# Kernel optimization log

Measured on AMD Instinct MI355X. Metric: run time of the kernel, lower is better.

Reference implementation:

```python
import jax, jax.numpy as jnp
import numpy as np

HEADS = 8
DIM_HEAD = 8  # TransMIL passes heads as dim_head to NystromLayer
INNER = HEADS * DIM_HEAD  # 64
LANDMARKS = 256
PINV_ITERS = 6
HID = 512
IN_DIM = 1024
N_TOKENS = 19600


def layernorm(x, g, b, eps=1e-5):
    mu = x.mean(-1, keepdims=True)
    var = ((x - mu) ** 2).mean(-1, keepdims=True)
    return (x - mu) / jnp.sqrt(var + eps) * g + b


def moore_penrose_pinv(a, iters=PINV_ITERS):
    # a: [b, h, m, m]
    abs_a = jnp.abs(a)
    z = jnp.swapaxes(a, -1, -2) / (jnp.max(abs_a.sum(-1)) * jnp.max(abs_a.sum(-2)))
    I = jnp.eye(a.shape[-1], dtype=a.dtype)
    for _ in range(iters):
        az = a @ z
        z = 0.25 * z @ (13.0 * I - az @ (15.0 * I - az @ (7.0 * I - az)))
    return z


def dwconv2d(x, w, b, pad_h, pad_w):
    # x: [B,C,H,W], w: [C,1,kh,kw] depthwise
    y = jax.lax.conv_general_dilated(
        x, w, (1, 1), [(pad_h, pad_h), (pad_w, pad_w)],
        dimension_numbers=('NCHW', 'OIHW', 'NCHW'), feature_group_count=x.shape[1])
    if b is not None:
        y = y + b[None, :, None, None]
    return y


def nystrom_attention(x, qkv_w, out_w, out_b, res_w):
    b, n, _ = x.shape
    m = LANDMARKS
    pad = (m - n % m) % m
    xp = jnp.pad(x, ((0, 0), (pad, 0), (0, 0)))  # pad at the FRONT (as in lucidrains)
    n_p = n + pad
    qkv = xp @ qkv_w  # [b, n_p, 3*inner]
    q, k, v = jnp.split(qkv, 3, axis=-1)
    to_heads = lambda t: t.reshape(b, n_p, HEADS, DIM_HEAD).transpose(0, 2, 1, 3)
    q, k, v = to_heads(q), to_heads(k), to_heads(v)  # [b,h,n_p,d]
    q = q * (DIM_HEAD ** -0.5)
    l = n_p // m  # segment length per landmark
    q_l = q.reshape(b, HEADS, m, l, DIM_HEAD).mean(3)  # [b,h,m,d]
    k_l = k.reshape(b, HEADS, m, l, DIM_HEAD).mean(3)
    attn1 = jax.nn.softmax(jnp.einsum('bhid,bhjd->bhij', q, k_l), -1)    # [b,h,n_p,m]
    attn2 = jax.nn.softmax(jnp.einsum('bhid,bhjd->bhij', q_l, k_l), -1)  # [b,h,m,m]
    attn3 = jax.nn.softmax(jnp.einsum('bhid,bhjd->bhij', q_l, k), -1)    # [b,h,m,n_p]
    out = (attn1 @ moore_penrose_pinv(attn2)) @ (attn3 @ v)  # [b,h,n_p,d]
    # residual depthwise conv over sequence dim: Conv2d(heads, heads, (33,1), padding=(16,0), groups=heads)
    out = out + dwconv2d(v, res_w, None, 16, 0)
    out = out.transpose(0, 2, 1, 3).reshape(b, n_p, INNER)
    out = out @ out_w + out_b
    return out[:, -n:]


def ppeg(x, H, W, w7, b7, w5, b5, w3, b3):
    B, _, C = x.shape
    cls, feat = x[:, :1], x[:, 1:]
    f = feat.transpose(0, 2, 1).reshape(B, C, H, W)
    y = f + dwconv2d(f, w7, b7, 3, 3) + dwconv2d(f, w5, b5, 2, 2) + dwconv2d(f, w3, b3, 1, 1)
    y = y.reshape(B, C, H * W).transpose(0, 2, 1)
    return jnp.concatenate([cls, y], axis=1)


def transmil_forward(x, fc1_w, fc1_b, cls_token,
                     l1_norm_g, l1_norm_b, l1_qkv_w, l1_out_w, l1_out_b, l1_res_w,
                     l2_norm_g, l2_norm_b, l2_qkv_w, l2_out_w, l2_out_b, l2_res_w,
                     ppeg7_w, ppeg7_b, ppeg5_w, ppeg5_b, ppeg3_w, ppeg3_b,
                     norm_g, norm_b):
    h = jax.nn.gelu(x @ fc1_w + fc1_b, approximate=False)  # [1, N, HID]
    N = h.shape[1]
    side = int(np.ceil(np.sqrt(N)))
    add = side * side - N
    h = jnp.concatenate([h, h[:, :add]], axis=1)
    cls = jnp.broadcast_to(cls_token, (h.shape[0], 1, h.shape[2]))
    h = jnp.concatenate([cls, h], axis=1)
    h = h + nystrom_attention(layernorm(h, l1_norm_g, l1_norm_b), l1_qkv_w, l1_out_w, l1_out_b, l1_res_w)
    h = ppeg(h, side, side, ppeg7_w, ppeg7_b, ppeg5_w, ppeg5_b, ppeg3_w, ppeg3_b)
    h = h + nystrom_attention(layernorm(h, l2_norm_g, l2_norm_b), l2_qkv_w, l2_out_w, l2_out_b, l2_res_w)
    return layernorm(h, norm_g, norm_b)[:, 0]  # [1, HID]


def setup_inputs() -> dict:
    key = jax.random.key(0)
    ks = jax.random.split(key, 16)
    s = 0.02
    inp = {
        'x': jax.random.normal(ks[0], (1, N_TOKENS, IN_DIM), jnp.float32),
        'fc1_w': jax.random.normal(ks[1], (IN_DIM, HID), jnp.float32) * s,
        'fc1_b': jnp.zeros((HID,), jnp.float32),
        'cls_token': jax.random.normal(ks[2], (1, 1, HID), jnp.float32),
        'l1_norm_g': jnp.ones((HID,), jnp.float32),
        'l1_norm_b': jnp.zeros((HID,), jnp.float32),
        'l1_qkv_w': jax.random.normal(ks[3], (HID, 3 * INNER), jnp.float32) * s,
        'l1_out_w': jax.random.normal(ks[4], (INNER, HID), jnp.float32) * s,
        'l1_out_b': jnp.zeros((HID,), jnp.float32),
        'l1_res_w': jax.random.normal(ks[5], (HEADS, 1, 33, 1), jnp.float32) * 0.05,
        'l2_norm_g': jnp.ones((HID,), jnp.float32),
        'l2_norm_b': jnp.zeros((HID,), jnp.float32),
        'l2_qkv_w': jax.random.normal(ks[6], (HID, 3 * INNER), jnp.float32) * s,
        'l2_out_w': jax.random.normal(ks[7], (INNER, HID), jnp.float32) * s,
        'l2_out_b': jnp.zeros((HID,), jnp.float32),
        'l2_res_w': jax.random.normal(ks[8], (HEADS, 1, 33, 1), jnp.float32) * 0.05,
        'ppeg7_w': jax.random.normal(ks[9], (HID, 1, 7, 7), jnp.float32) * 0.05,
        'ppeg7_b': jnp.zeros((HID,), jnp.float32),
        'ppeg5_w': jax.random.normal(ks[10], (HID, 1, 5, 5), jnp.float32) * 0.05,
        'ppeg5_b': jnp.zeros((HID,), jnp.float32),
        'ppeg3_w': jax.random.normal(ks[11], (HID, 1, 3, 3), jnp.float32) * 0.05,
        'ppeg3_b': jnp.zeros((HID,), jnp.float32),
        'norm_g': jnp.ones((HID,), jnp.float32),
        'norm_b': jnp.zeros((HID,), jnp.float32),
    }
    return inp


def reference(x, fc1_w, fc1_b, cls_token,
              l1_norm_g, l1_norm_b, l1_qkv_w, l1_out_w, l1_out_b, l1_res_w,
              l2_norm_g, l2_norm_b, l2_qkv_w, l2_out_w, l2_out_b, l2_res_w,
              ppeg7_w, ppeg7_b, ppeg5_w, ppeg5_b, ppeg3_w, ppeg3_b,
              norm_g, norm_b):
    return transmil_forward(x, fc1_w, fc1_b, cls_token,
                            l1_norm_g, l1_norm_b, l1_qkv_w, l1_out_w, l1_out_b, l1_res_w,
                            l2_norm_g, l2_norm_b, l2_qkv_w, l2_out_w, l2_out_b, l2_res_w,
                            ppeg7_w, ppeg7_b, ppeg5_w, ppeg5_b, ppeg3_w, ppeg3_b,
                            norm_g, norm_b)
```

## Files before the change

### kernel.cpp

```cpp
#include <hip/hip_runtime.h>

namespace {

constexpr int NP   = 19712;
constexpr int NT   = 19601;
constexpr int NPIX = 19600;
constexpr int HD   = 512;
constexpr int ID   = 1024;
constexpr int NH   = 8;
constexpr int DH   = 8;
constexpr int NL   = 256;
constexpr int PADR = 111;
constexpr int SIDE = 140;
constexpr int A3CHK = 256;
constexpr int A3NB  = NP / A3CHK;

constexpr int PTW = 16, PTH = 16, PCC = 16;
constexpr int PHW = PTW + 6, PHH = PTH + 6;
constexpr int PSLOT = 20;

typedef __attribute__((ext_vector_type(8))) short bf16x8;
typedef __attribute__((ext_vector_type(4))) float f32x4;

#define F4MAD(a, s, v) { (a).x += (s)*(v).x; (a).y += (s)*(v).y; (a).z += (s)*(v).z; (a).w += (s)*(v).w; }
#define F4FMA(a, ww, v) { (a).x += (ww).x*(v).x; (a).y += (ww).y*(v).y; (a).z += (ww).z*(v).z; (a).w += (ww).w*(v).w; }

#define GLOAD16(gptr, lptr) \
    __builtin_amdgcn_global_load_lds((const __attribute__((address_space(1))) void*)(gptr), \
                                     (__attribute__((address_space(3))) void*)(lptr), 16, 0, 0)

__device__ inline short f2bf(float f) {
    union { float f; unsigned u; } v; v.f = f;
    unsigned r = v.u + 0x7fffu + ((v.u >> 16) & 1u);
    return (short)(r >> 16);
}

__global__ void castX(const float* __restrict__ src, short* __restrict__ dst)
{
    size_t c = (size_t)blockIdx.x * 256 + threadIdx.x;
    const float4 x0 = *(const float4*)&src[c * 8];
    const float4 x1 = *(const float4*)&src[c * 8 + 4];
    bf16x8 p;
    p[0] = f2bf(x0.x); p[1] = f2bf(x0.y); p[2] = f2bf(x0.z); p[3] = f2bf(x0.w);
    p[4] = f2bf(x1.x); p[5] = f2bf(x1.y); p[6] = f2bf(x1.z); p[7] = f2bf(x1.w);
    *(bf16x8*)&dst[c * 8] = p;
}

__global__ void castT(const float* __restrict__ src, short* __restrict__ dst, int R, int C)
{
    __shared__ float t[32][33];
    const int tx = threadIdx.x & 31, ty = threadIdx.x >> 5;
    const int c0 = blockIdx.x * 32, r0 = blockIdx.y * 32;
    #pragma unroll
    for (int j = 0; j < 4; ++j)
        t[ty + 8 * j][tx] = src[(size_t)(r0 + ty + 8 * j) * C + c0 + tx];
    __syncthreads();
    #pragma unroll
    for (int j = 0; j < 4; ++j)
        dst[(size_t)(c0 + ty + 8 * j) * R + r0 + tx] = f2bf(t[tx][ty + 8 * j]);
}

__global__ __launch_bounds__(256) void gemm_fc1(const short* __restrict__ Xb,
                                                const short* __restrict__ Wt,
                                                const float* __restrict__ bias,
                                                float* __restrict__ out)
{
    __shared__ __align__(16) short As[2][128 * 32];
    __shared__ __align__(16) short Bs[2][128 * 32];
    const int tid  = threadIdx.x;
    const int col0 = blockIdx.x * 128;
    const int row0 = blockIdx.y * 128;
    const int wave = tid >> 6, lane = tid & 63;
    const int quad = lane >> 4, l16 = lane & 15;
    const int m_base = (wave >> 1) * 64, n_base = (wave & 1) * 64;
    const int kch = (quad ^ ((l16 >> 1) & 3)) * 8;
    f32x4 acc[4][4] = {};

    int    aldo[2];
    size_t agoff[2], bgoff[2];
    #pragma unroll
    for (int i = 0; i < 2; ++i) {
        int slot = i * 256 + wave * 64 + lane;
        int row  = slot >> 2;
        int g    = (slot & 3) ^ ((slot >> 3) & 3);
        aldo[i]  = slot * 8;
        agoff[i] = (size_t)(row0 + row) * ID + g * 8;
        bgoff[i] = (size_t)(col0 + row) * ID + g * 8;
    }
    auto stage = [&](int b, int k0) {
        #pragma unroll
        for (int i = 0; i < 2; ++i) {
            GLOAD16(&Xb[agoff[i] + k0], &As[b][aldo[i]]);
            GLOAD16(&Wt[bgoff[i] + k0], &Bs[b][aldo[i]]);
        }
    };

    stage(0, 0);
    __syncthreads();
    #pragma unroll 1
    for (int t = 0; t < 32; ++t) {
        const int cur = t & 1;
        if (t < 31) stage(cur ^ 1, (t + 1) * 32);
        bf16x8 af[4], bfr[4];
        #pragma unroll
        for (int i = 0; i < 4; ++i) {
            af[i]  = *(const bf16x8*)&As[cur][(m_base + i * 16 + l16) * 32 + kch];
            bfr[i] = *(const bf16x8*)&Bs[cur][(n_base + i * 16 + l16) * 32 + kch];
        }
        #pragma unroll
        for (int mi = 0; mi < 4; ++mi)
            #pragma unroll
            for (int ni = 0; ni < 4; ++ni)
                acc[mi][ni] = __builtin_amdgcn_mfma_f32_16x16x32_bf16(af[mi], bfr[ni], acc[mi][ni], 0, 0, 0);
        __syncthreads();
    }
    #pragma unroll
    for (int mi = 0; mi < 4; ++mi) {
        #pragma unroll
        for (int r = 0; r < 4; ++r) {
            int gr = row0 + m_base + mi * 16 + quad * 4 + r;
            if (gr >= NPIX) continue;
            #pragma unroll
            for (int ni = 0; ni < 4; ++ni) {
                int gc = col0 + n_base + ni * 16 + l16;
                float v = acc[mi][ni][r] + bias[gc];
                v = 0.5f * v * (1.f + erff(v * 0.70710678118654752f));
                out[(size_t)(gr + 1) * HD + gc] = v;
            }
        }
    }
}

__global__ __launch_bounds__(256) void gemm_qkv(const short* __restrict__ xpB,
                                                const short* __restrict__ Wt,
                                                float* __restrict__ qh,
                                                float* __restrict__ kh,
                                                float* __restrict__ vh)
{
    __shared__ __align__(16) short As[2][128 * 32];
    __shared__ __align__(16) short Bs[2][64 * 32];
    const int tid  = threadIdx.x;
    const int col0 = blockIdx.x * 64;
    const int row0 = blockIdx.y * 128;
    const int wave = tid >> 6, lane = tid & 63;
    const int quad = lane >> 4, l16 = lane & 15;
    const int m_base = (wave >> 1) * 64, n_base = (wave & 1) * 32;
    const int kch = (quad ^ ((l16 >> 1) & 3)) * 8;
    f32x4 acc[4][2] = {};

    int    aldo[2];
    size_t agoff[2];
    #pragma unroll
    for (int i = 0; i < 2; ++i) {
        int slot = i * 256 + wave * 64 + lane;
        int row  = slot >> 2;
        int g    = (slot & 3) ^ ((slot >> 3) & 3);
        aldo[i]  = slot * 8;
        agoff[i] = (size_t)(row0 + row) * HD + g * 8;
    }
    int bldo; size_t bgoff;
    {
        int slot = wave * 64 + lane;
        int row  = slot >> 2;
        int g    = (slot & 3) ^ ((slot >> 3) & 3);
        bldo  = slot * 8;
        bgoff = (size_t)(col0 + row) * HD + g * 8;
    }
    auto stage = [&](int b, int k0) {
        #pragma unroll
        for (int i = 0; i < 2; ++i)
            GLOAD16(&xpB[agoff[i] + k0], &As[b][aldo[i]]);
        GLOAD16(&Wt[bgoff + k0], &Bs[b][bldo]);
    };

    stage(0, 0);
    __syncthreads();
    #pragma unroll 1
    for (int t = 0; t < 16; ++t) {
        const int cur = t & 1;
        if (t < 15) stage(cur ^ 1, (t + 1) * 32);
        bf16x8 af[4], bfr[2];
        #pragma unroll
        for (int i = 0; i < 4; ++i)
            af[i] = *(const bf16x8*)&As[cur][(m_base + i * 16 + l16) * 32 + kch];
        #pragma unroll
        for (int i = 0; i < 2; ++i)
            bfr[i] = *(const bf16x8*)&Bs[cur][(n_base + i * 16 + l16) * 32 + kch];
        #pragma unroll
        for (int mi = 0; mi < 4; ++mi)
            #pragma unroll
            for (int ni = 0; ni < 2; ++ni)
                acc[mi][ni] = __builtin_amdgcn_mfma_f32_16x16x32_bf16(af[mi], bfr[ni], acc[mi][ni], 0, 0, 0);
        __syncthreads();
    }
    const int which = blockIdx.x;
    float* dst = (which == 0) ? qh : (which == 1) ? kh : vh;
    const float scale = (which == 0) ? 0.35355339059327373f : 1.f;
    #pragma unroll
    for (int mi = 0; mi < 4; ++mi) {
        #pragma unroll
        for (int r = 0; r < 4; ++r) {
            int gr = row0 + m_base + mi * 16 + quad * 4 + r;
            #pragma unroll
            for (int ni = 0; ni < 2; ++ni) {
                int n = n_base + ni * 16 + l16;
                int hh = n >> 3, d = n & 7;
                dst[((size_t)hh * NP + gr) * DH + d] = acc[mi][ni][r] * scale;
            }
        }
    }
}

__global__ void cls_init(const float* __restrict__ cls, float* __restrict__ h)
{
    int t = blockIdx.x * 256 + threadIdx.x;
    if (t < HD) h[t] = cls[t];
}

__global__ void copy512(const float* __restrict__ src, float* __restrict__ dst)
{
    dst[threadIdx.x] = src[threadIdx.x];
}

__global__ __launch_bounds__(256) void ln_pad(const float* __restrict__ h,
                                              const float* __restrict__ g,
                                              const float* __restrict__ b,
                                              short* __restrict__ xp)
{
    const int wave = threadIdx.x >> 6, lane = threadIdx.x & 63;
    const int row = blockIdx.x * 4 + wave;
    short* dst = xp + (size_t)row * HD + lane * 8;
    if (row < PADR) {
        bf16x8 z = {};
        *(bf16x8*)dst = z;
        return;
    }
    const float* src = h + (size_t)(row - PADR) * HD + lane * 8;
    float4 v0 = *(const float4*)src;
    float4 v1 = *(const float4*)(src + 4);
    float v[8] = {v0.x, v0.y, v0.z, v0.w, v1.x, v1.y, v1.z, v1.w};
    float s = 0.f;
    #pragma unroll
    for (int i = 0; i < 8; ++i) s += v[i];
    #pragma unroll
    for (int o = 1; o < 64; o <<= 1) s += __shfl_xor(s, o);
    float mu = s * (1.f / HD);
    float ss = 0.f;
    #pragma unroll
    for (int i = 0; i < 8; ++i) { float d = v[i] - mu; ss += d * d; }
    #pragma unroll
    for (int o = 1; o < 64; o <<= 1) ss += __shfl_xor(ss, o);
    float inv = rsqrtf(ss * (1.f / HD) + 1e-5f);
    float4 g0 = *(const float4*)&g[lane * 8];
    float4 g1 = *(const float4*)&g[lane * 8 + 4];
    float4 b0 = *(const float4*)&b[lane * 8];
    float4 b1 = *(const float4*)&b[lane * 8 + 4];
    float gg[8] = {g0.x, g0.y, g0.z, g0.w, g1.x, g1.y, g1.z, g1.w};
    float bb[8] = {b0.x, b0.y, b0.z, b0.w, b1.x, b1.y, b1.z, b1.w};
    bf16x8 o;
    #pragma unroll
    for (int i = 0; i < 8; ++i) o[i] = f2bf((v[i] - mu) * inv * gg[i] + bb[i]);
    *(bf16x8*)dst = o;
}

__global__ void landmarks(const float* __restrict__ qh, const float* __restrict__ kh,
                          float* __restrict__ ql, float* __restrict__ kl)
{
    int idx = blockIdx.x * 256 + threadIdx.x;
    int sel = idx >> 14;
    int rem = idx & 16383;
    int h = rem >> 11;
    int i = (rem >> 3) & 255;
    int d = rem & 7;
    const float* src = sel ? kh : qh;
    size_t base = ((size_t)h * NP + (size_t)i * 77) * DH + d;
    float s = 0.f;
    for (int j = 0; j < 77; ++j) s += src[base + (size_t)j * DH];
    (sel ? kl : ql)[((size_t)h * NL + i) * DH + d] = s * (1.f / 77.f);
}

__global__ void attn2_softmax(const float* __restrict__ ql, const float* __restrict__ kl,
                              float* __restrict__ a)
{
    const int i = blockIdx.x, h = blockIdx.y, j = threadIdx.x;
    __shared__ float sq[8];
    __shared__ float red[256];
    if (j < 8) sq[j] = ql[((size_t)h * NL + i) * DH + j];
    __syncthreads();
    const float* kr = kl + ((size_t)h * NL + j) * DH;
    float s = 0.f;
    #pragma unroll
    for (int d = 0; d < 8; ++d) s += sq[d] * kr[d];
    float e = __expf(s);
    red[j] = e;
    __syncthreads();
    for (int off = 128; off > 0; off >>= 1) {
        if (j < off) red[j] += red[j + off];
        __syncthreads();
    }
    a[((size_t)h * NL + i) * NL + j] = e / red[0];
}

__global__ void pinv_norms(const float* __restrict__ a, float* __restrict__ part)
{
    const int h = blockIdx.x & 7;
    const int mode = blockIdx.x >> 3;
    const int tid = threadIdx.x;
    const float* ah = a + (size_t)h * NL * NL;
    float s = 0.f;
    if (mode == 0) { for (int j = 0; j < NL; ++j) s += fabsf(ah[tid * NL + j]); }
    else           { for (int i = 0; i < NL; ++i) s += fabsf(ah[i * NL + tid]); }
    __shared__ float red[256];
    red[tid] = s;
    __syncthreads();
    for (int off = 128; off > 0; off >>= 1) {
        if (tid < off) red[tid] = fmaxf(red[tid], red[tid + off]);
        __syncthreads();
    }
    if (tid == 0) part[mode * 8 + h] = red[0];
}

__global__ void z0_init(const float* __restrict__ a, const float* __restrict__ part,
                        float* __restrict__ z)
{
    float s1 = part[0], s2 = part[8];
    #pragma unroll
    for (int h = 1; h < 8; ++h) { s1 = fmaxf(s1, part[h]); s2 = fmaxf(s2, part[8 + h]); }
    float inv = 1.f / (s1 * s2);
    int idx = blockIdx.x * 256 + threadIdx.x;
    int h = idx >> 16;
    int rem = idx & 65535;
    int i = rem >> 8, j = rem & 255;
    z[idx] = a[((size_t)h * NL + j) * NL + i] * inv;
}

__global__ void mm256(const float* __restrict__ A, const float* __restrict__ B,
                      float* __restrict__ D)
{
    const int h = blockIdx.z;
    const float* Ah = A + (size_t)h * NL * NL;
    const float* Bh = B + (size_t)h * NL * NL;
    float* Dh = D + (size_t)h * NL * NL;
    __shared__ __align__(16) float As[16][36];
    __shared__ __align__(16) float Bs[16][68];
    const int tid = threadIdx.x;
    const int tx = tid & 15, ty = tid >> 4;
    const int row0 = blockIdx.x * 32;
    const int col0 = blockIdx.y * 64;
    float acc[2][4] = {};
    const int ar = tid >> 3;
    const int ak = (tid & 7) * 2;
    const int bk = tid >> 4;
    const int bj = (tid & 15) * 4;
    for (int k0 = 0; k0 < NL; k0 += 16) {
        float2 av = *(const float2*)&Ah[(size_t)(row0 + ar) * NL + k0 + ak];
        As[ak][ar] = av.x; As[ak + 1][ar] = av.y;
        *(float4*)&Bs[bk][bj] = *(const float4*)&Bh[(size_t)(k0 + bk) * NL + col0 + bj];
        __syncthreads();
        #pragma unroll
        for (int k = 0; k < 16; ++k) {
            float2 a = *(const float2*)&As[k][ty * 2];
            float4 b = *(const float4*)&Bs[k][tx * 4];
            acc[0][0] += a.x * b.x; acc[0][1] += a.x * b.y; acc[0][2] += a.x * b.z; acc[0][3] += a.x * b.w;
            acc[1][0] += a.y * b.x; acc[1][1] += a.y * b.y; acc[1][2] += a.y * b.z; acc[1][3] += a.y * b.w;
        }
        __syncthreads();
    }
    #pragma unroll
    for (int r = 0; r < 2; ++r) {
        int gr = row0 + ty * 2 + r;
        #pragma unroll
        for (int c = 0; c < 4; ++c)
            Dh[(size_t)gr * NL + col0 + tx * 4 + c] = acc[r][c];
    }
}

__global__ __launch_bounds__(256) void mmF(const float* __restrict__ S,
                                           const float* __restrict__ w,
                                           float* __restrict__ wn,
                                           const float* __restrict__ yin,
                                           float* __restrict__ yout)
{
    const int h = blockIdx.z;
    const int tid = threadIdx.x;
    if (blockIdx.y == 4) {
        __shared__ float yL[NL * 9];
        __shared__ float tL[NL * 9];
        __shared__ float uL[NL * 9];
        const int s = blockIdx.x;
        const float* yh = yin + (size_t)h * NL * DH;
        #pragma unroll
        for (int i = 0; i < 8; ++i) {
            int idx = tid + 256 * i;
            yL[(idx >> 3) * 9 + (idx & 7)] = yh[idx];
        }
        __syncthreads();
        const float* wr = w + ((size_t)h * NL + tid) * NL;
        float t1[8] = {};
        for (int j = 0; j < NL; j += 4) {
            float4 wv = *(const float4*)&wr[j];
            #pragma unroll
            for (int d = 0; d < 8; ++d)
                t1[d] += wv.x * yL[j * 9 + d] + wv.y * yL[(j + 1) * 9 + d]
                       + wv.z * yL[(j + 2) * 9 + d] + wv.w * yL[(j + 3) * 9 + d];
        }
        #pragma unroll
        for (int d = 0; d < 8; ++d) {
            tL[tid * 9 + d] = t1[d];
            uL[tid * 9 + d] = 7.f * yL[tid * 9 + d] - t1[d];
        }
        __syncthreads();
        const int r = s * 32 + (tid >> 3), d = tid & 7;
        const float* Sr = S + ((size_t)h * NL + r) * NL;
        float acc = 13.f * yL[r * 9 + d] - 15.f * tL[r * 9 + d];
        for (int j = 0; j < NL; j += 4) {
            float4 sv = *(const float4*)&Sr[j];
            acc += sv.x * uL[j * 9 + d] + sv.y * uL[(j + 1) * 9 + d]
                 + sv.z * uL[(j + 2) * 9 + d] + sv.w * uL[(j + 3) * 9 + d];
        }
        yout[((size_t)h * NL + r) * DH + d] = acc;
        return;
    }
    const float* Sh = S + (size_t)h * NL * NL;
    const float* wh = w + (size_t)h * NL * NL;
    float* Dh = wn + (size_t)h * NL * NL;
    __shared__ __align__(16) float As[16][36];
    __shared__ __align__(16) float Bs[16][68];
    const int tx = tid & 15, ty = tid >> 4;
    const int row0 = blockIdx.x * 32;
    const int col0 = blockIdx.y * 64;
    float acc[2][4] = {};
    const int ar = tid >> 3;
    const int ak = (tid & 7) * 2;
    const int bk = tid >> 4;
    const int bj = (tid & 15) * 4;
    for (int k0 = 0; k0 < NL; k0 += 16) {
        float2 av = *(const float2*)&Sh[(size_t)(row0 + ar) * NL + k0 + ak];
        As[ak][ar] = av.x; As[ak + 1][ar] = av.y;
        size_t bo = (size_t)(k0 + bk) * NL + col0 + bj;
        float4 bw = *(const float4*)&wh[bo];
        float4 bs = *(const float4*)&Sh[bo];
        Bs[bk][bj]     = 7.f * bw.x - bs.x;
        Bs[bk][bj + 1] = 7.f * bw.y - bs.y;
        Bs[bk][bj + 2] = 7.f * bw.z - bs.z;
        Bs[bk][bj + 3] = 7.f * bw.w - bs.w;
        __syncthreads();
        #pragma unroll
        for (int k = 0; k < 16; ++k) {
            float2 a = *(const float2*)&As[k][ty * 2];
            float4 b = *(const float4*)&Bs[k][tx * 4];
            acc[0][0] += a.x * b.x; acc[0][1] += a.x * b.y; acc[0][2] += a.x * b.z; acc[0][3] += a.x * b.w;
            acc[1][0] += a.y * b.x; acc[1][1] += a.y * b.y; acc[1][2] += a.y * b.z; acc[1][3] += a.y * b.w;
        }
        __syncthreads();
    }
    #pragma unroll
    for (int r = 0; r < 2; ++r) {
        int gr = row0 + ty * 2 + r;
        #pragma unroll
        for (int c = 0; c < 4; ++c) {
            int gc = col0 + tx * 4 + c;
            size_t o = (size_t)gr * NL + gc;
            Dh[o] = 0.25f * (13.f * wh[o] - 15.f * Sh[o] + acc[r][c]);
        }
    }
}

__global__ __launch_bounds__(256) void yiter(const float* __restrict__ w,
                                             const float* __restrict__ S,
                                             const float* __restrict__ yin,
                                             float* __restrict__ yout)
{
    const int s = blockIdx.x, h = blockIdx.y, tid = threadIdx.x;
    __shared__ float yL[NL * 9];
    __shared__ float tL[NL * 9];
    __shared__ float uL[NL * 9];
    const float* yh = yin + (size_t)h * NL * DH;
    #pragma unroll
    for (int i = 0; i < 8; ++i) {
        int idx = tid + 256 * i;
        yL[(idx >> 3) * 9 + (idx & 7)] = yh[idx];
    }
    __syncthreads();
    const float* wr = w + ((size_t)h * NL + tid) * NL;
    float t1[8] = {};
    for (int j = 0; j < NL; j += 4) {
        float4 wv = *(const float4*)&wr[j];
        #pragma unroll
        for (int d = 0; d < 8; ++d)
            t1[d] += wv.x * yL[j * 9 + d] + wv.y * yL[(j + 1) * 9 + d]
                   + wv.z * yL[(j + 2) * 9 + d] + wv.w * yL[(j + 3) * 9 + d];
    }
    #pragma unroll
    for (int d = 0; d < 8; ++d) {
        tL[tid * 9 + d] = t1[d];
        uL[tid * 9 + d] = 7.f * yL[tid * 9 + d] - t1[d];
    }
    __syncthreads();
    const int r = s * 32 + (tid >> 3), d = tid & 7;
    const float* Sr = S + ((size_t)h * NL + r) * NL;
    float acc = 13.f * yL[r * 9 + d] - 15.f * tL[r * 9 + d];
    for (int j = 0; j < NL; j += 4) {
        float4 sv = *(const float4*)&Sr[j];
        acc += sv.x * uL[j * 9 + d] + sv.y * uL[(j + 1) * 9 + d]
             + sv.z * uL[(j + 2) * 9 + d] + sv.w * uL[(j + 3) * 9 + d];
    }
    yout[((size_t)h * NL + r) * DH + d] = acc;
}

__global__ void polyv(const float* __restrict__ M, const float* __restrict__ vin,
                      float* __restrict__ vout, float scale)
{
    const int h = blockIdx.y;
    __shared__ float vs[NL * DH];
    const int tid = threadIdx.x;
    const float* vh = vin + (size_t)h * NL * DH;
    #pragma unroll
    for (int i = 0; i < 8; ++i) vs[tid + 256 * i] = vh[tid + 256 * i];
    __syncthreads();
    const int row = blockIdx.x * 32 + (tid >> 3);
    const int d = tid & 7;
    const float* Mr = M + ((size_t)h * NL + row) * NL;
    float acc = 0.f;
    #pragma unroll 4
    for (int j = 0; j < NL; j += 4) {
        float4 m = *(const float4*)&Mr[j];
        acc += m.x * vs[j * 8 + d]      + m.y * vs[j * 8 + 8 + d]
             + m.z * vs[j * 8 + 16 + d] + m.w * vs[j * 8 + 24 + d];
    }
    vout[((size_t)h * NL + row) * DH + d] = acc * scale;
}

__global__ __launch_bounds__(256) void attn3v(const float* __restrict__ kh,
                                              const float* __restrict__ vh,
                                              const float* __restrict__ ql,
                                              float* __restrict__ part)
{
    const int ck = blockIdx.x, h = blockIdx.y, tid = threadIdx.x;
    __shared__ __align__(16) float4 kv[A3CHK][4];
    const float* kb = kh + ((size_t)h * NP + (size_t)ck * A3CHK) * DH;
    const float* vb = vh + ((size_t)h * NP + (size_t)ck * A3CHK) * DH;
    #pragma unroll
    for (int i = 0; i < 2; ++i) {
        int idx = tid + 256 * i;
        int t = idx >> 1, p = idx & 1;
        kv[t][p]     = *(const float4*)&kb[t * 8 + p * 4];
        kv[t][2 + p] = *(const float4*)&vb[t * 8 + p * 4];
    }
    float q[8];
    const float* qp = ql + ((size_t)h * NL + tid) * DH;
    #pragma unroll
    for (int d = 0; d < 8; ++d) q[d] = qp[d];
    __syncthreads();
    float den = 0.f;
    float4 a0 = make_float4(0.f, 0.f, 0.f, 0.f);
    float4 a1 = make_float4(0.f, 0.f, 0.f, 0.f);
    #pragma unroll 4
    for (int t = 0; t < A3CHK; ++t) {
        float4 k0 = kv[t][0], k1 = kv[t][1];
        float s = q[0] * k0.x + q[1] * k0.y + q[2] * k0.z + q[3] * k0.w
                + q[4] * k1.x + q[5] * k1.y + q[6] * k1.z + q[7] * k1.w;
        float e = __expf(s);
        den += e;
        float4 v0 = kv[t][2], v1 = kv[t][3];
        F4MAD(a0, e, v0); F4MAD(a1, e, v1);
    }
    float* p = part + (((size_t)h * A3NB + ck) * NL + tid) * 9;
    p[0] = den;
    p[1] = a0.x; p[2] = a0.y; p[3] = a0.z; p[4] = a0.w;
    p[5] = a1.x; p[6] = a1.y; p[7] = a1.z; p[8] = a1.w;
}

__global__ void attn3v_merge(const float* __restrict__ part, float* __restrict__ y)
{
    const int h = blockIdx.x;
    const int i = blockIdx.y * 32 + (threadIdx.x >> 3);
    const int d = threadIdx.x & 7;
    float acc = 0.f, den = 0.f;
    const float* p = part + ((size_t)h * A3NB * NL + i) * 9;
    for (int ck = 0; ck < A3NB; ++ck) {
        const float* q = p + (size_t)ck * NL * 9;
        den += q[0];
        acc += q[1 + d];
    }
    y[((size_t)h * NL + i) * DH + d] = acc / den;
}

__global__ __launch_bounds__(256) void attn1_conv(const float* __restrict__ qh,
                                                  const float* __restrict__ vh,
                                                  const float* __restrict__ klg,
                                                  const float* __restrict__ zwg,
                                                  const float* __restrict__ rw,
                                                  float* __restrict__ aout)
{
    const int h = blockIdx.y;
    __shared__ __align__(16) float kl[NL * DH];
    __shared__ __align__(16) float zw[NL * DH];
    const int tid = threadIdx.x;
    #pragma unroll
    for (int q = 0; q < 8; ++q) {
        kl[tid + 256 * q] = klg[(size_t)h * NL * DH + tid + 256 * q];
        zw[tid + 256 * q] = zwg[(size_t)h * NL * DH + tid + 256 * q];
    }
    __syncthreads();
    const int r = blockIdx.x * 256 + tid;
    if (r >= NT) return;
    const int t = r + PADR;
    const float* qp = qh + ((size_t)h * NP + t) * DH;
    float4 q0 = *(const float4*)qp;
    float4 q1 = *(const float4*)(qp + 4);
    float den = 0.f;
    float4 acc0 = make_float4(0.f, 0.f, 0.f, 0.f);
    float4 acc1 = make_float4(0.f, 0.f, 0.f, 0.f);
    #pragma unroll 4
    for (int i = 0; i < NL; ++i) {
        float4 k0 = *(const float4*)&kl[i * 8];
        float4 k1 = *(const float4*)&kl[i * 8 + 4];
        float s = q0.x * k0.x + q0.y * k0.y + q0.z * k0.z + q0.w * k0.w
                + q1.x * k1.x + q1.y * k1.y + q1.z * k1.z + q1.w * k1.w;
        float e = __expf(s);
        den += e;
        float4 z0 = *(const float4*)&zw[i * 8];
        float4 z1 = *(const float4*)&zw[i * 8 + 4];
        F4MAD(acc0, e, z0); F4MAD(acc1, e, z1);
    }
    float inv = 1.f / den;
    const float* vb = vh + (size_t)h * NP * DH;
    float4 c0 = make_float4(0.f, 0.f, 0.f, 0.f);
    float4 c1 = make_float4(0.f, 0.f, 0.f, 0.f);
    #pragma unroll
    for (int j = 0; j < 33; ++j) {
        int tp = t - 16 + j;
        if (tp >= NP) continue;
        float wv = rw[h * 33 + j];
        float4 v0 = *(const float4*)&vb[(size_t)tp * 8];
        float4 v1 = *(const float4*)&vb[(size_t)tp * 8 + 4];
        F4MAD(c0, wv, v0); F4MAD(c1, wv, v1);
    }
    float* op = aout + (size_t)r * 64 + h * 8;
    *(float4*)op = make_float4(acc0.x * inv + c0.x, acc0.y * inv + c0.y,
                               acc0.z * inv + c0.z, acc0.w * inv + c0.w);
    *(float4*)(op + 4) = make_float4(acc1.x * inv + c1.x, acc1.y * inv + c1.y,
                                     acc1.z * inv + c1.z, acc1.w * inv + c1.w);
}

__global__ void outproj(const float* __restrict__ aout, const float* __restrict__ W,
                        const float* __restrict__ bias, float* __restrict__ h)
{
    const int r0 = blockIdx.x * 16;
    const int tid = threadIdx.x;
    __shared__ float ao[16][64];
    #pragma unroll
    for (int s = 0; s < 2; ++s) {
        int idx = tid + s * 512;
        int rr = idx >> 6, kk = idx & 63;
        int gr = r0 + rr;
        ao[rr][kk] = (gr < NT) ? aout[(size_t)gr * 64 + kk] : 0.f;
    }
    __syncthreads();
    float acc[16] = {};
    for (int k = 0; k < 64; ++k) {
        float wv = W[(size_t)k * HD + tid];
        #pragma unroll
        for (int r = 0; r < 16; ++r) acc[r] += ao[r][k] * wv;
    }
    float bv = bias[tid];
    #pragma unroll
    for (int r = 0; r < 16; ++r) {
        int gr = r0 + r;
        if (gr < NT) h[(size_t)gr * HD + tid] += acc[r] + bv;
    }
}

__global__ void ppeg_wprep(const float* __restrict__ w7, const float* __restrict__ b7,
                           const float* __restrict__ w5, const float* __restrict__ b5,
                           const float* __restrict__ w3, const float* __restrict__ b3,
                           float* __restrict__ wc, float* __restrict__ bsum)
{
    int idx = blockIdx.x * 256 + threadIdx.x;
    if (idx < HD * 49) {
        int c = idx / 49, t = idx - c * 49;
        int dy = t / 7 - 3, dx = t % 7 - 3;
        float v = w7[idx];
        if (dy >= -2 && dy <= 2 && dx >= -2 && dx <= 2) v += w5[c * 25 + (dy + 2) * 5 + (dx + 2)];
        if (dy >= -1 && dy <= 1 && dx >= -1 && dx <= 1) v += w3[c * 9 + (dy + 1) * 3 + (dx + 1)];
        if (t == 24) v += 1.f;
        wc[idx] = v;
    } else if (idx < HD * 49 + HD) {
        int c = idx - HD * 49;
        bsum[c] = b7[c] + b5[c] + b3[c];
    }
}

__global__ __launch_bounds__(256) void ppeg_direct(const float* __restrict__ hin,
                                                   const float* __restrict__ wc,
                                                   const float* __restrict__ bsum,
                                                   float* __restrict__ hout)
{
    __shared__ __align__(16) float in_sh[PHH * PHW * PSLOT];
    __shared__ float wL[49 * PCC];
    const int tid = threadIdx.x;
    const int tx0 = blockIdx.x * PTW;
    const int ty0 = blockIdx.y * PTH;
    const int c0  = blockIdx.z * PCC;
    for (int i = tid; i < 49 * PCC; i += 256) {
        int c = i / 49, tap = i - c * 49;
        wL[tap * PCC + c] = wc[(size_t)(c0 + c) * 49 + tap];
    }
    for (int idx = tid; idx < PHH * PHW * 4; idx += 256) {
        int pos = idx >> 2, q = idx & 3;
        int ly = pos / PHW, lx = pos - ly * PHW;
        int gy = ty0 - 3 + ly, gx = tx0 - 3 + lx;
        float4 v = make_float4(0.f, 0.f, 0.f, 0.f);
        if (gy >= 0 && gy < SIDE && gx >= 0 && gx < SIDE)
            v = *(const float4*)&hin[(size_t)(1 + gy * SIDE + gx) * HD + c0 + q * 4];
        *(float4*)&in_sh[pos * PSLOT + q * 4] = v;
    }
    __syncthreads();
    const int y  = tid >> 4;
    const int x4 = (tid >> 2) & 3;
    const int c4 = tid & 3;
    const int xb = x4 * 4;
    float4 acc[4] = {make_float4(0.f,0.f,0.f,0.f), make_float4(0.f,0.f,0.f,0.f),
                     make_float4(0.f,0.f,0.f,0.f), make_float4(0.f,0.f,0.f,0.f)};
    #pragma unroll 1
    for (int dy = 0; dy < 7; ++dy) {
        float4 row[10];
        #pragma unroll
        for (int k = 0; k < 10; ++k)
            row[k] = *(const float4*)&in_sh[((y + dy) * PHW + xb + k) * PSLOT + c4 * 4];
        #pragma unroll
        for (int dx = 0; dx < 7; ++dx) {
            float4 wv = *(const float4*)&wL[(dy * 7 + dx) * PCC + c4 * 4];
            #pragma unroll
            for (int xi = 0; xi < 4; ++xi) F4FMA(acc[xi], wv, row[xi + dx]);
        }
    }
    const int gy = ty0 + y;
    if (gy >= SIDE) return;
    float4 bv = *(const float4*)&bsum[c0 + c4 * 4];
    #pragma unroll
    for (int xi = 0; xi < 4; ++xi) {
        int gx = tx0 + xb + xi;
        if (gx >= SIDE) continue;
        float4 o = make_float4(acc[xi].x + bv.x, acc[xi].y + bv.y,
                               acc[xi].z + bv.z, acc[xi].w + bv.w);
        *(float4*)&hout[(size_t)(1 + gy * SIDE + gx) * HD + c0 + c4 * 4] = o;
    }
}

__global__ void final_ln(const float* __restrict__ h, const float* __restrict__ g,
                         const float* __restrict__ b, float* __restrict__ out)
{
    const int tid = threadIdx.x;
    float v0 = h[tid], v1 = h[tid + 256];
    __shared__ float red[256];
    red[tid] = v0 + v1;
    __syncthreads();
    for (int off = 128; off > 0; off >>= 1) {
        if (tid < off) red[tid] += red[tid + off];
        __syncthreads();
    }
    float mu = red[0] * (1.f / HD);
    __syncthreads();
    float d0 = v0 - mu, d1 = v1 - mu;
    red[tid] = d0 * d0 + d1 * d1;
    __syncthreads();
    for (int off = 128; off > 0; off >>= 1) {
        if (tid < off) red[tid] += red[tid + off];
        __syncthreads();
    }
    float inv = rsqrtf(red[0] * (1.f / HD) + 1e-5f);
    out[tid]       = d0 * inv * g[tid] + b[tid];
    out[tid + 256] = d1 * inv * g[tid + 256] + b[tid + 256];
}

}

extern "C" void kernel_launch(void* const* d_in, const int* in_sizes, int n_in,
                              void* d_out, int out_size, void* d_ws, size_t ws_size,
                              hipStream_t stream)
{
    const float* x      = (const float*)d_in[0];
    const float* fc1_w  = (const float*)d_in[1];
    const float* fc1_b  = (const float*)d_in[2];
    const float* cls    = (const float*)d_in[3];
    const float* l1_g   = (const float*)d_in[4];
    const float* l1_bb  = (const float*)d_in[5];
    const float* l1_qkv = (const float*)d_in[6];
    const float* l1_ow  = (const float*)d_in[7];
    const float* l1_ob  = (const float*)d_in[8];
    const float* l1_rw  = (const float*)d_in[9];
    const float* l2_g   = (const float*)d_in[10];
    const float* l2_bb  = (const float*)d_in[11];
    const float* l2_qkv = (const float*)d_in[12];
    const float* l2_ow  = (const float*)d_in[13];
    const float* l2_ob  = (const float*)d_in[14];
    const float* l2_rw  = (const float*)d_in[15];
    const float* p7w    = (const float*)d_in[16];
    const float* p7b    = (const float*)d_in[17];
    const float* p5w    = (const float*)d_in[18];
    const float* p5b    = (const float*)d_in[19];
    const float* p3w    = (const float*)d_in[20];
    const float* p3b    = (const float*)d_in[21];
    const float* ng     = (const float*)d_in[22];
    const float* nb     = (const float*)d_in[23];
    float* out = (float*)d_out;

    char* ws = (char*)d_ws;
    size_t off = 0;
    auto alloc = [&](size_t bytes) {
        char* p = ws + off;
        off += (bytes + 255) & ~(size_t)255;
        return (void*)p;
    };
    float* bufA = (float*)alloc((size_t)NP * HD * 4);
    float* bufB = (float*)alloc((size_t)NP * HD * 4);
    float* qh   = (float*)alloc((size_t)NH * NP * DH * 4);
    float* kh   = (float*)alloc((size_t)NH * NP * DH * 4);
    float* vh   = (float*)alloc((size_t)NH * NP * DH * 4);
    float* aout = (float*)alloc((size_t)NP * 64 * 4);
    float* ql   = (float*)alloc((size_t)NH * NL * DH * 4);
    float* klm  = (float*)alloc((size_t)NH * NL * DH * 4);
    float* ybuf = (float*)alloc((size_t)NH * NL * DH * 4);
    float* ybuf2= (float*)alloc((size_t)NH * NL * DH * 4);
    float* zwb  = (float*)alloc((size_t)NH * NL * DH * 4);
    float* a2   = (float*)alloc((size_t)NH * NL * NL * 4);
    float* zb0  = (float*)alloc((size_t)NH * NL * NL * 4);
    float* azb  = (float*)alloc((size_t)NH * NL * NL * 4);
    float* tb   = (float*)alloc((size_t)NH * NL * NL * 4);
    float* ub   = (float*)alloc((size_t)NH * NL * NL * 4);
    float* part = (float*)alloc(256);
    float* a3p  = (float*)alloc((size_t)NH * A3NB * NL * 9 * 4);
    float* wcomb = (float*)alloc((size_t)HD * 49 * 4);
    float* bsum  = (float*)alloc((size_t)HD * 4);
    short* wt1   = (short*)alloc((size_t)HD * ID * 2);
    short* wtq   = (short*)alloc((size_t)192 * HD * 2);
    short* xb    = (short*)alloc((size_t)NP * ID * 2);
    short* xpB   = (short*)alloc((size_t)NP * HD * 2);
    (void)ws_size; (void)in_sizes; (void)n_in; (void)out_size;

    castX<<<(NPIX * ID / 8) / 256, 256, 0, stream>>>(x, xb);
    castT<<<dim3(HD / 32, ID / 32), 256, 0, stream>>>(fc1_w, wt1, ID, HD);
    gemm_fc1<<<dim3(4, 154), 256, 0, stream>>>(xb, wt1, fc1_b, bufA);
    cls_init<<<2, 256, 0, stream>>>(cls, bufA);

    auto attention = [&](float* hbuf, const float* lg, const float* lb,
                         const float* qkvw, const float* ow, const float* ob,
                         const float* rw) {
        ln_pad<<<NP / 4, 256, 0, stream>>>(hbuf, lg, lb, xpB);
        castT<<<dim3(192 / 32, HD / 32), 256, 0, stream>>>(qkvw, wtq, HD, 192);
        gemm_qkv<<<dim3(3, 154), 256, 0, stream>>>(xpB, wtq, qh, kh, vh);
        landmarks<<<128, 256, 0, stream>>>(qh, kh, ql, klm);
        attn2_softmax<<<dim3(NL, NH), 256, 0, stream>>>(ql, klm, a2);
        pinv_norms<<<16, 256, 0, stream>>>(a2, part);
        z0_init<<<2048, 256, 0, stream>>>(a2, part, zb0);
        attn3v<<<dim3(A3NB, NH), 256, 0, stream>>>(kh, vh, ql, a3p);
        attn3v_merge<<<dim3(NH, 8), 256, 0, stream>>>(a3p, ybuf);
        mm256<<<dim3(8, 4, 8), 256, 0, stream>>>(a2, zb0, azb);
        float* wc = azb;
        float* wn = tb;
        float* yc = ybuf;
        float* yn = ybuf2;
        for (int it = 0; it < 6; ++it) {
            mm256<<<dim3(8, 4, 8), 256, 0, stream>>>(wc, wc, ub);
            if (it < 5) {
                mmF<<<dim3(8, 5, 8), 256, 0, stream>>>(ub, wc, wn, yc, yn);
                { float* t = yc; yc = yn; yn = t; }
                { float* t = wc; wc = wn; wn = t; }
            } else {
                yiter<<<dim3(8, 8), 256, 0, stream>>>(wc, ub, yc, yn);
                { float* t = yc; yc = yn; yn = t; }
            }
        }
        polyv<<<dim3(8, NH), 256, 0, stream>>>(zb0, yc, zwb, 2.44140625e-4f);
        attn1_conv<<<dim3(77, NH), 256, 0, stream>>>(qh, vh, klm, zwb, rw, aout);
        outproj<<<(NT + 15) / 16, 512, 0, stream>>>(aout, ow, ob, hbuf);
    };

    attention(bufA, l1_g, l1_bb, l1_qkv, l1_ow, l1_ob, l1_rw);

    ppeg_wprep<<<(HD * 49 + HD + 255) / 256, 256, 0, stream>>>(p7w, p7b, p5w, p5b, p3w, p3b,
                                                               wcomb, bsum);
    copy512<<<1, 512, 0, stream>>>(bufA, bufB);
    ppeg_direct<<<dim3((SIDE + PTW - 1) / PTW, (SIDE + PTH - 1) / PTH, HD / PCC),
                  256, 0, stream>>>(bufA, wcomb, bsum, bufB);

    attention(bufB, l2_g, l2_bb, l2_qkv, l2_ow, l2_ob, l2_rw);
    final_ln<<<1, 256, 0, stream>>>(bufB, ng, nb, out);
}
```

Measured before the change: 1.032 ms.

## Retile QKV GEMM over all outputs and fold pinv init transpose into consumers

The QKV projection GEMM now has each block cover 64 rows and all 192 output columns, so each activation tile is read once instead of three times. The pseudo-inverse setup drops the explicit transposed z0 matrix. It assumes softmax rows sum to one and are non-negative, so only column sums are needed for the scale. The first a·z product and the final polynomial-vector step read attn2 transposed directly. This removes one kernel launch and a 2 MB buffer round trip, at the cost of strided reads in polyvT and a possible register-pressure increase in the GEMM.

Result: no change. 1.021 ms (-1.0%).

```diff
diff --git a/kernel.cpp b/kernel.cpp
--- a/kernel.cpp
+++ b/kernel.cpp
@@ -137,40 +137,40 @@
                                                 float* __restrict__ kh,
                                                 float* __restrict__ vh)
 {
-    __shared__ __align__(16) short As[2][128 * 32];
-    __shared__ __align__(16) short Bs[2][64 * 32];
+    __shared__ __align__(16) short As[2][64 * 32];
+    __shared__ __align__(16) short Bs[2][192 * 32];
     const int tid  = threadIdx.x;
-    const int col0 = blockIdx.x * 64;
-    const int row0 = blockIdx.y * 128;
+    const int row0 = blockIdx.x * 64;
     const int wave = tid >> 6, lane = tid & 63;
     const int quad = lane >> 4, l16 = lane & 15;
-    const int m_base = (wave >> 1) * 64, n_base = (wave & 1) * 32;
+    const int m_base = (wave & 1) * 32;
+    const int n_base = (wave >> 1) * 96;
     const int kch = (quad ^ ((l16 >> 1) & 3)) * 8;
-    f32x4 acc[4][2] = {};
-
-    int    aldo[2];
-    size_t agoff[2];
-    #pragma unroll
-    for (int i = 0; i < 2; ++i) {
-        int slot = i * 256 + wave * 64 + lane;
+    f32x4 acc[2][6] = {};
+
+    int aldo; size_t agoff;
+    {
+        int slot = tid;
         int row  = slot >> 2;
         int g    = (slot & 3) ^ ((slot >> 3) & 3);
-        aldo[i]  = slot * 8;
-        agoff[i] = (size_t)(row0 + row) * HD + g * 8;
-    }
-    int bldo; size_t bgoff;
-    {
-        int slot = wave * 64 + lane;
+        aldo  = slot * 8;
+        agoff = (size_t)(row0 + row) * HD + g * 8;
+    }
+    int    bldo[3];
+    size_t bgoff[3];
+    #pragma unroll
+    for (int i = 0; i < 3; ++i) {
+        int slot = i * 256 + tid;
         int row  = slot >> 2;
         int g    = (slot & 3) ^ ((slot >> 3) & 3);
-        bldo  = slot * 8;
-        bgoff = (size_t)(col0 + row) * HD + g * 8;
+        bldo[i]  = slot * 8;
+        bgoff[i] = (size_t)row * HD + g * 8;
     }
     auto stage = [&](int b, int k0) {
-        #pragma unroll
-        for (int i = 0; i < 2; ++i)
-            GLOAD16(&xpB[agoff[i] + k0], &As[b][aldo[i]]);
-        GLOAD16(&Wt[bgoff + k0], &Bs[b][bldo]);
+        GLOAD16(&xpB[agoff + k0], &As[b][aldo]);
+        #pragma unroll
+        for (int i = 0; i < 3; ++i)
+            GLOAD16(&Wt[bgoff[i] + k0], &Bs[b][bldo[i]]);
     };
 
     stage(0, 0);
@@ -179,33 +179,34 @@
     for (int t = 0; t < 16; ++t) {
         const int cur = t & 1;
         if (t < 15) stage(cur ^ 1, (t + 1) * 32);
-        bf16x8 af[4], bfr[2];
-        #pragma unroll
-        for (int i = 0; i < 4; ++i)
+        bf16x8 af[2], bfr[6];
+        #pragma unroll
+        for (int i = 0; i < 2; ++i)
             af[i] = *(const bf16x8*)&As[cur][(m_base + i * 16 + l16) * 32 + kch];
         #pragma unroll
-        for (int i = 0; i < 2; ++i)
+        for (int i = 0; i < 6; ++i)
             bfr[i] = *(const bf16x8*)&Bs[cur][(n_base + i * 16 + l16) * 32 + kch];
         #pragma unroll
-        for (int mi = 0; mi < 4; ++mi)
+        for (int mi = 0; mi < 2; ++mi)
             #pragma unroll
-            for (int ni = 0; ni < 2; ++ni)
+            for (int ni = 0; ni < 6; ++ni)
                 acc[mi][ni] = __builtin_amdgcn_mfma_f32_16x16x32_bf16(af[mi], bfr[ni], acc[mi][ni], 0, 0, 0);
         __syncthreads();
     }
-    const int which = blockIdx.x;
-    float* dst = (which == 0) ? qh : (which == 1) ? kh : vh;
-    const float scale = (which == 0) ? 0.35355339059327373f : 1.f;
-    #pragma unroll
-    for (int mi = 0; mi < 4; ++mi) {
+    #pragma unroll
+    for (int mi = 0; mi < 2; ++mi) {
         #pragma unroll
         for (int r = 0; r < 4; ++r) {
             int gr = row0 + m_base + mi * 16 + quad * 4 + r;
             #pragma unroll
-            for (int ni = 0; ni < 2; ++ni) {
+            for (int ni = 0; ni < 6; ++ni) {
                 int n = n_base + ni * 16 + l16;
-                int hh = n >> 3, d = n & 7;
-                dst[((size_t)hh * NP + gr) * DH + d] = acc[mi][ni][r] * scale;
+                int which = n >> 6;
+                int nn = n & 63;
+                int hh = nn >> 3, d = nn & 7;
+                float* dst = (which == 0) ? qh : (which == 1) ? kh : vh;
+                float scl  = (which == 0) ? 0.35355339059327373f : 1.f;
+                dst[((size_t)hh * NP + gr) * DH + d] = acc[mi][ni][r] * scl;
             }
         }
     }
@@ -303,13 +304,11 @@
 
 __global__ void pinv_norms(const float* __restrict__ a, float* __restrict__ part)
 {
-    const int h = blockIdx.x & 7;
-    const int mode = blockIdx.x >> 3;
+    const int h = blockIdx.x;
     const int tid = threadIdx.x;
     const float* ah = a + (size_t)h * NL * NL;
     float s = 0.f;
-    if (mode == 0) { for (int j = 0; j < NL; ++j) s += fabsf(ah[tid * NL + j]); }
-    else           { for (int i = 0; i < NL; ++i) s += fabsf(ah[i * NL + tid]); }
+    for (int i = 0; i < NL; ++i) s += ah[(size_t)i * NL + tid];
     __shared__ float red[256];
     red[tid] = s;
     __syncthreads();
@@ -317,21 +316,53 @@
         if (tid < off) red[tid] = fmaxf(red[tid], red[tid + off]);
         __syncthreads();
     }
-    if (tid == 0) part[mode * 8 + h] = red[0];
-}
-
-__global__ void z0_init(const float* __restrict__ a, const float* __restrict__ part,
-                        float* __restrict__ z)
-{
-    float s1 = part[0], s2 = part[8];
-    #pragma unroll
-    for (int h = 1; h < 8; ++h) { s1 = fmaxf(s1, part[h]); s2 = fmaxf(s2, part[8 + h]); }
-    float inv = 1.f / (s1 * s2);
-    int idx = blockIdx.x * 256 + threadIdx.x;
-    int h = idx >> 16;
-    int rem = idx & 65535;
-    int i = rem >> 8, j = rem & 255;
-    z[idx] = a[((size_t)h * NL + j) * NL + i] * inv;
+    if (tid == 0) part[h] = red[0];
+}
+
+__global__ void mm256T(const float* __restrict__ A, const float* __restrict__ part,
+                       float* __restrict__ D)
+{
+    const int h = blockIdx.z;
+    const float* Ah = A + (size_t)h * NL * NL;
+    float* Dh = D + (size_t)h * NL * NL;
+    float mx = part[0];
+    #pragma unroll
+    for (int i = 1; i < 8; ++i) mx = fmaxf(mx, part[i]);
+    const float inv = 1.f / mx;
+    __shared__ __align__(16) float As[16][36];
+    __shared__ __align__(16) float Bs[16][68];
+    const int tid = threadIdx.x;
+    const int tx = tid & 15, ty = tid >> 4;
+    const int row0 = blockIdx.x * 32;
+    const int col0 = blockIdx.y * 64;
+    float acc[2][4] = {};
+    const int ar = tid >> 3;
+    const int ak = (tid & 7) * 2;
+    const int jr = tid >> 2;
+    const int kc = (tid & 3) * 4;
+    for (int k0 = 0; k0 < NL; k0 += 16) {
+        float2 av = *(const float2*)&Ah[(size_t)(row0 + ar) * NL + k0 + ak];
+        As[ak][ar] = av.x; As[ak + 1][ar] = av.y;
+        float4 bv = *(const float4*)&Ah[(size_t)(col0 + jr) * NL + k0 + kc];
+        Bs[kc][jr] = bv.x; Bs[kc + 1][jr] = bv.y;
+        Bs[kc + 2][jr] = bv.z; Bs[kc + 3][jr] = bv.w;
+        __syncthreads();
+        #pragma unroll
+        for (int k = 0; k < 16; ++k) {
+            float2 a = *(const float2*)&As[k][ty * 2];
+            float4 b = *(const float4*)&Bs[k][tx * 4];
+            acc[0][0] += a.x * b.x; acc[0][1] += a.x * b.y; acc[0][2] += a.x * b.z; acc[0][3] += a.x * b.w;
+            acc[1][0] += a.y * b.x; acc[1][1] += a.y * b.y; acc[1][2] += a.y * b.z; acc[1][3] += a.y * b.w;
+        }
+        __syncthreads();
+    }
+    #pragma unroll
+    for (int r = 0; r < 2; ++r) {
+        int gr = row0 + ty * 2 + r;
+        #pragma unroll
+        for (int c = 0; c < 4; ++c)
+            Dh[(size_t)gr * NL + col0 + tx * 4 + c] = inv * acc[r][c];
+    }
 }
 
 __global__ void mm256(const float* __restrict__ A, const float* __restrict__ B,
@@ -508,8 +539,8 @@
     yout[((size_t)h * NL + r) * DH + d] = acc;
 }
 
-__global__ void polyv(const float* __restrict__ M, const float* __restrict__ vin,
-                      float* __restrict__ vout, float scale)
+__global__ void polyvT(const float* __restrict__ A, const float* __restrict__ part,
+                       const float* __restrict__ vin, float* __restrict__ vout)
 {
     const int h = blockIdx.y;
     __shared__ float vs[NL * DH];
@@ -518,16 +549,16 @@
     #pragma unroll
     for (int i = 0; i < 8; ++i) vs[tid + 256 * i] = vh[tid + 256 * i];
     __syncthreads();
+    float mx = part[0];
+    #pragma unroll
+    for (int i = 1; i < 8; ++i) mx = fmaxf(mx, part[i]);
+    const float scale = 2.44140625e-4f / mx;
     const int row = blockIdx.x * 32 + (tid >> 3);
     const int d = tid & 7;
-    const float* Mr = M + ((size_t)h * NL + row) * NL;
+    const float* Ah = A + (size_t)h * NL * NL;
     float acc = 0.f;
-    #pragma unroll 4
-    for (int j = 0; j < NL; j += 4) {
-        float4 m = *(const float4*)&Mr[j];
-        acc += m.x * vs[j * 8 + d]      + m.y * vs[j * 8 + 8 + d]
-             + m.z * vs[j * 8 + 16 + d] + m.w * vs[j * 8 + 24 + d];
-    }
+    for (int j = 0; j < NL; ++j)
+        acc += Ah[(size_t)j * NL + row] * vs[j * 8 + d];
     vout[((size_t)h * NL + row) * DH + d] = acc * scale;
 }
 
@@ -826,7 +857,6 @@
     float* ybuf2= (float*)alloc((size_t)NH * NL * DH * 4);
     float* zwb  = (float*)alloc((size_t)NH * NL * DH * 4);
     float* a2   = (float*)alloc((size_t)NH * NL * NL * 4);
-    float* zb0  = (float*)alloc((size_t)NH * NL * NL * 4);
     float* azb  = (float*)alloc((size_t)NH * NL * NL * 4);
     float* tb   = (float*)alloc((size_t)NH * NL * NL * 4);
     float* ub   = (float*)alloc((size_t)NH * NL * NL * 4);
@@ -850,14 +880,13 @@
                          const float* rw) {
         ln_pad<<<NP / 4, 256, 0, stream>>>(hbuf, lg, lb, xpB);
         castT<<<dim3(192 / 32, HD / 32), 256, 0, stream>>>(qkvw, wtq, HD, 192);
-        gemm_qkv<<<dim3(3, 154), 256, 0, stream>>>(xpB, wtq, qh, kh, vh);
+        gemm_qkv<<<NP / 64, 256, 0, stream>>>(xpB, wtq, qh, kh, vh);
         landmarks<<<128, 256, 0, stream>>>(qh, kh, ql, klm);
         attn2_softmax<<<dim3(NL, NH), 256, 0, stream>>>(ql, klm, a2);
-        pinv_norms<<<16, 256, 0, stream>>>(a2, part);
-        z0_init<<<2048, 256, 0, stream>>>(a2, part, zb0);
+        pinv_norms<<<8, 256, 0, stream>>>(a2, part);
         attn3v<<<dim3(A3NB, NH), 256, 0, stream>>>(kh, vh, ql, a3p);
         attn3v_merge<<<dim3(NH, 8), 256, 0, stream>>>(a3p, ybuf);
-        mm256<<<dim3(8, 4, 8), 256, 0, stream>>>(a2, zb0, azb);
+        mm256T<<<dim3(8, 4, 8), 256, 0, stream>>>(a2, part, azb);
         float* wc = azb;
         float* wn = tb;
         float* yc = ybuf;
@@ -873,7 +902,7 @@
                 { float* t = yc; yc = yn; yn = t; }
             }
         }
-        polyv<<<dim3(8, NH), 256, 0, stream>>>(zb0, yc, zwb, 2.44140625e-4f);
+        polyvT<<<dim3(8, NH), 256, 0, stream>>>(a2, part, yc, zwb);
         attn1_conv<<<dim3(77, NH), 256, 0, stream>>>(qh, vh, klm, zwb, rw, aout);
         outproj<<<(NT + 15) / 16, 512, 0, stream>>>(aout, ow, ob, hbuf);
     };
```
